# Optimization experiments

Measured on AMD Instinct MI355X. Metric: run time of the kernel, lower is better.

## Reference

```python
import jax, jax.numpy as jnp
import numpy as np

WL = 8  # word length passed to block_quantize_nearest


def block_quantize_nearest(x, wl=WL):
    """QPyTorch block_quantize_nearest with dim=0.

    One shared exponent per row (block = row of x.view(N, -1)).
    Equivalent math to the CUDA kernel: base exponent e = floor(log2(max|row|)),
    quantization step = 2^(e + 2 - wl), round-half-up in the rebased bit space.
    """
    flat = x.reshape(x.shape[0], -1)
    max_abs = jnp.max(jnp.abs(flat), axis=1, keepdims=True)  # [N, 1]
    tiny = jnp.asarray(np.finfo(np.float32).tiny, x.dtype)
    exp = jnp.floor(jnp.log2(jnp.maximum(max_abs, tiny)))
    step = jnp.exp2(exp + 2.0 - wl)                          # [N, 1]
    q = jnp.floor(flat / step + 0.5) * step                  # round-half-up
    q = jnp.where(max_abs > 0, q, flat)                      # all-zero rows pass through
    return q.reshape(x.shape)


def setup_inputs() -> dict:
    key = jax.random.key(0)
    k1, k2, k3 = jax.random.split(key, 3)
    B, D_IN, D_OUT = 8192, 4096, 4096
    x = jax.random.normal(k1, (B, D_IN), dtype=jnp.float32)
    # nn.Linear init scale ~ 1/sqrt(fan_in)
    W = jax.random.normal(k2, (D_OUT, D_IN), dtype=jnp.float32) * (1.0 / np.sqrt(D_IN))
    b = jax.random.normal(k3, (D_OUT,), dtype=jnp.float32) * (1.0 / np.sqrt(D_IN))
    return {"x": x, "W": W, "b": b}


def reference(x, W, b):
    # Linear: y = x @ W^T + b  (x already 2D, flatten(1) is identity)
    h = jnp.einsum('bi,oi->bo', x.reshape(x.shape[0], -1), W) + b
    q = block_quantize_nearest(h, WL)
    return jax.nn.relu(q)
```

## Files before the change

### kernel.cpp

```cpp
#include <hip/hip_runtime.h>

#define M 8192
#define N 4096
#define K 4096
#define BM 256
#define BN 256
#define BK 64
#define NKT (K / BK)
#define NIT (NKT / 2)

typedef __attribute__((ext_vector_type(8))) short bf16x8;
typedef __attribute__((ext_vector_type(4))) short bf16x4;
typedef __attribute__((ext_vector_type(4))) float f32x4;
typedef __attribute__((address_space(1))) const unsigned GU;
typedef __attribute__((address_space(3))) unsigned LU;

__device__ __forceinline__ unsigned short f2bf(float f) {
    unsigned u = __float_as_uint(f);
    u += 0x7fffu + ((u >> 16) & 1u);
    return (unsigned short)(u >> 16);
}

__global__ __launch_bounds__(256) void cvt_bf16_2(
    const float* __restrict__ s1, unsigned short* __restrict__ d1, int n1_4,
    const float* __restrict__ s2, unsigned short* __restrict__ d2, int n2_4,
    int* __restrict__ rowmax)
{
    if (blockIdx.x < 32) rowmax[(blockIdx.x << 8) | threadIdx.x] = 0;

    const int span = gridDim.x * blockDim.x;
    const int tid  = blockIdx.x * blockDim.x + threadIdx.x;
    const int total = n1_4 + n2_4;

    for (int base = tid; base < total; base += 4 * span) {
        f32x4 v[4];
        #pragma unroll
        for (int j = 0; j < 4; ++j) {
            const int i = base + j * span;
            const f32x4* p = (i < n1_4) ? ((const f32x4*)s1) + i
                                        : ((const f32x4*)s2) + (i - n1_4);
            v[j] = *p;
        }
        #pragma unroll
        for (int j = 0; j < 4; ++j) {
            const int i = base + j * span;
            bf16x4 o;
            #pragma unroll
            for (int k = 0; k < 4; ++k) o[k] = (short)f2bf(v[j][k]);
            bf16x4* q = (i < n1_4) ? ((bf16x4*)d1) + i : ((bf16x4*)d2) + (i - n1_4);
            *q = o;
        }
    }
}

#define BAR()   __builtin_amdgcn_s_barrier()
#define LGKM0() do { asm volatile("s_waitcnt lgkmcnt(0)" ::: "memory"); \
                     __builtin_amdgcn_sched_barrier(0); } while (0)
#define LGKM8() asm volatile("s_waitcnt lgkmcnt(8)" ::: "memory")
#define VM6()   asm volatile("s_waitcnt vmcnt(6)" ::: "memory")

#define QUAD(AR, BR, MOFF, NOFF)                                               \
    do {                                                                       \
        __builtin_amdgcn_s_setprio(1);                                         \
        _Pragma("unroll")                                                      \
        for (int m_ = 0; m_ < 4; ++m_) {                                       \
            _Pragma("unroll")                                                  \
            for (int n_ = 0; n_ < 2; ++n_) {                                   \
                acc[MOFF + m_][NOFF + n_] =                                    \
                    __builtin_amdgcn_mfma_f32_16x16x32_bf16(                   \
                        AR[m_][0], BR[n_][0], acc[MOFF + m_][NOFF + n_], 0, 0, 0); \
                acc[MOFF + m_][NOFF + n_] =                                    \
                    __builtin_amdgcn_mfma_f32_16x16x32_bf16(                   \
                        AR[m_][1], BR[n_][1], acc[MOFF + m_][NOFF + n_], 0, 0, 0); \
            }                                                                  \
        }                                                                      \
        __builtin_amdgcn_s_setprio(0);                                         \
    } while (0)

__global__ __launch_bounds__(512, 2) void gemm_bf16(
    const unsigned short* __restrict__ xb, const unsigned short* __restrict__ wb,
    const float* __restrict__ bias, float* __restrict__ out,
    int* __restrict__ rowmax)
{
    __shared__ __align__(16) short smem[65536];

    const int bid = blockIdx.x;
    const int tm = bid % (M / BM);
    const int tn = bid / (M / BM);
    const int bm = tm * BM, bn = tn * BN;

    const int t    = threadIdx.x;
    const int w_id = t >> 6;
    const int l    = t & 63;
    const int wr   = w_id >> 2;
    const int wc   = w_id & 3;
    const int lr   = l & 15;
    const int g    = l >> 4;

    const int srow_l = l >> 2;
    const int scol_l = ((l & 3) * 8) ^ ((l >> 5) * 16);
    const int loff = lr * 32 + ((g * 8) ^ ((lr >> 3) << 4));

    auto stageA = [&](int buf, int h, int kt) {
        #pragma unroll
        for (int j = 0; j < 2; ++j) {
            const int s = w_id * 2 + j;
            const unsigned short* gp =
                xb + (size_t)(bm + h * 128 + (s >> 1) * 16 + srow_l) * K
                   + kt * 64 + (s & 1) * 32 + scol_l;
            __builtin_amdgcn_global_load_lds(
                (const GU*)gp, (LU*)&smem[buf * 16384 + h * 8192 + s * 512], 16, 0, 0);
        }
    };
    auto stageB = [&](int buf, int h, int kt) {
        #pragma unroll
        for (int j = 0; j < 2; ++j) {
            const int s = w_id * 2 + j;
            const unsigned short* gp =
                wb + (size_t)(bn + h * 128 + (s >> 1) * 16 + srow_l) * K
                   + kt * 64 + (s & 1) * 32 + scol_l;
            __builtin_amdgcn_global_load_lds(
                (const GU*)gp, (LU*)&smem[32768 + buf * 16384 + h * 8192 + s * 512], 16, 0, 0);
        }
    };
    auto ldA = [&](int buf, int m, int ks) -> bf16x8 {
        return *(const bf16x8*)&smem[buf * 16384 + wr * 8192 + (m * 2 + ks) * 512 + loff];
    };
    auto ldB = [&](int buf, int n, int ks) -> bf16x8 {
        return *(const bf16x8*)&smem[32768 + buf * 16384 + (wc >> 1) * 8192 +
                                     (((wc & 1) * 4 + n) * 2 + ks) * 512 + loff];
    };

    f32x4 acc[8][4];
    #pragma unroll
    for (int m = 0; m < 8; ++m)
        #pragma unroll
        for (int n = 0; n < 4; ++n)
            acc[m][n] = (f32x4){0.f, 0.f, 0.f, 0.f};

    bf16x8 a03[4][2], a47[4][2], b01[2][2], b23[2][2];

    stageB(0, 0, 0); stageB(0, 1, 0); stageA(0, 0, 0); stageA(0, 1, 0);
    stageB(1, 0, 1); stageB(1, 1, 1); stageA(1, 0, 1);
    VM6();
    BAR();

    for (int it = 0; it < NIT; ++it) {
        const int t1  = 2 * it + 1;
        const int tp0 = (2 * it + 2) & (NKT - 1);
        const int tp1 = (2 * it + 3) & (NKT - 1);

        #pragma unroll
        for (int m = 0; m < 4; ++m) { a03[m][0] = ldA(0, m, 0); a03[m][1] = ldA(0, m, 1); }
        #pragma unroll
        for (int n = 0; n < 2; ++n) { b01[n][0] = ldB(0, n, 0); b01[n][1] = ldB(0, n, 1); }
        stageA(1, 1, t1);
        LGKM8();
        BAR(); LGKM0();
        QUAD(a03, b01, 0, 0);
        BAR();

        #pragma unroll
        for (int n = 0; n < 2; ++n) { b23[n][0] = ldB(0, 2 + n, 0); b23[n][1] = ldB(0, 2 + n, 1); }
        stageB(0, 0, tp0);
        BAR(); LGKM0();
        QUAD(a03, b23, 0, 2);
        BAR();

        #pragma unroll
        for (int m = 0; m < 4; ++m) { a47[m][0] = ldA(0, 4 + m, 0); a47[m][1] = ldA(0, 4 + m, 1); }
        stageB(0, 1, tp0);
        BAR(); LGKM0();
        QUAD(a47, b23, 4, 2);
        BAR();

        stageA(0, 0, tp0);
        BAR(); LGKM0();
        QUAD(a47, b01, 4, 0);
        VM6();
        BAR();

        #pragma unroll
        for (int m = 0; m < 4; ++m) { a03[m][0] = ldA(1, m, 0); a03[m][1] = ldA(1, m, 1); }
        #pragma unroll
        for (int n = 0; n < 2; ++n) { b01[n][0] = ldB(1, n, 0); b01[n][1] = ldB(1, n, 1); }
        stageA(0, 1, tp0);
        LGKM8();
        BAR(); LGKM0();
        QUAD(a03, b01, 0, 0);
        BAR();

        #pragma unroll
        for (int n = 0; n < 2; ++n) { b23[n][0] = ldB(1, 2 + n, 0); b23[n][1] = ldB(1, 2 + n, 1); }
        stageB(1, 0, tp1);
        BAR(); LGKM0();
        QUAD(a03, b23, 0, 2);
        BAR();

        #pragma unroll
        for (int m = 0; m < 4; ++m) { a47[m][0] = ldA(1, 4 + m, 0); a47[m][1] = ldA(1, 4 + m, 1); }
        stageB(1, 1, tp1);
        BAR(); LGKM0();
        QUAD(a47, b23, 4, 2);
        BAR();

        stageA(1, 0, tp1);
        BAR(); LGKM0();
        QUAD(a47, b01, 4, 0);
        VM6();
        BAR();
    }

    __syncthreads();

    float bv[4];
    #pragma unroll
    for (int n = 0; n < 4; ++n)
        bv[n] = bias[bn + wc * 64 + n * 16 + lr];

    #pragma unroll
    for (int m = 0; m < 8; ++m) {
        #pragma unroll
        for (int r = 0; r < 4; ++r) {
            const int row = bm + wr * 128 + m * 16 + g * 4 + r;
            float amax = 0.f;
            #pragma unroll
            for (int n = 0; n < 4; ++n) {
                acc[m][n][r] += bv[n];
                amax = fmaxf(amax, fabsf(acc[m][n][r]));
            }
            #pragma unroll
            for (int off = 1; off < 16; off <<= 1)
                amax = fmaxf(amax, __shfl_xor(amax, off));
            if (lr == 0)
                atomicMax(rowmax + row, __float_as_int(amax));
        }
    }

    float* hs = (float*)smem;
    #pragma unroll
    for (int p = 0; p < 2; ++p) {
        if (p) __syncthreads();
        if (wr == p) {
            #pragma unroll
            for (int m = 0; m < 8; ++m)
                #pragma unroll
                for (int r = 0; r < 4; ++r)
                    #pragma unroll
                    for (int n = 0; n < 4; ++n)
                        hs[(m * 16 + g * 4 + r) * 256 + wc * 64 + n * 16 + lr] =
                            acc[m][n][r];
        }
        __syncthreads();
        #pragma unroll
        for (int j = 0; j < 16; ++j) {
            const int fi  = j * 2048 + t * 4;
            const int row = fi >> 8;
            const int col = fi & 255;
            *(f32x4*)&out[(size_t)(bm + p * 128 + row) * N + bn + col] =
                *(const f32x4*)&hs[fi];
        }
    }
}

__global__ __launch_bounds__(256) void quant_relu(
    float* __restrict__ y, const int* __restrict__ rowmax)
{
    const int nvec = (M * N) / 4;
    const int span = gridDim.x * blockDim.x;
    const int tid  = blockIdx.x * blockDim.x + threadIdx.x;

    for (int base = tid; base < nvec; base += 4 * span) {
        f32x4 v[4];
        unsigned mb[4];
        #pragma unroll
        for (int j = 0; j < 4; ++j)
            v[j] = ((const f32x4*)y)[base + j * span];
        #pragma unroll
        for (int j = 0; j < 4; ++j)
            mb[j] = (unsigned)rowmax[(base + j * span) >> 10];
        #pragma unroll
        for (int j = 0; j < 4; ++j) {
            const unsigned eb   = mb[j] & 0x7f800000u;
            const float    step = __uint_as_float(eb - 0x03000000u);
            const float    inv  = __uint_as_float(0x82000000u - eb);
            f32x4 q;
            #pragma unroll
            for (int k = 0; k < 4; ++k) {
                const float qq = floorf(v[j][k] * inv + 0.5f) * step;
                q[k] = fmaxf(mb[j] ? qq : v[j][k], 0.f);
            }
            ((f32x4*)y)[base + j * span] = q;
        }
    }
}

extern "C" void kernel_launch(void* const* d_in, const int* in_sizes, int n_in,
                              void* d_out, int out_size, void* d_ws, size_t ws_size,
                              hipStream_t stream) {
    const float* x = (const float*)d_in[0];
    const float* w = (const float*)d_in[1];
    const float* b = (const float*)d_in[2];
    float* out = (float*)d_out;

    const size_t XB = (size_t)M * K * 2;
    const size_t WB = (size_t)N * K * 2;

    unsigned short* xb = (unsigned short*)d_ws;
    unsigned short* wb = (unsigned short*)((char*)d_ws + XB);
    int* rowmax        = (int*)((char*)d_ws + XB + WB);

    cvt_bf16_2<<<3072, 256, 0, stream>>>(x, xb, (M * K) / 4, w, wb, (N * K) / 4, rowmax);
    gemm_bf16<<<dim3((M / BM) * (N / BN)), 512, 0, stream>>>(xb, wb, b, out, rowmax);
    quant_relu<<<2048, 256, 0, stream>>>(out, rowmax);
}
```

Measured before the change: 532.2 us.

## Fuse quant-ReLU into GEMM via cooperative grid sync with two tiles per block

Replaces the separate GEMM and quant_relu launches with one cooperative kernel of 256 persistent blocks. Each block computes two N-tiles, stores the first, keeps the second in registers across a grid-wide sync, then quantizes the second in registers and re-reads only the first tile to quantize it. This removes one full read-modify-write pass over the 128 MB output and one launch. In exchange it adds a grid barrier, serializes two tiles per block, and rereads half the output.

```diff
diff --git a/kernel.cpp b/kernel.cpp
--- a/kernel.cpp
+++ b/kernel.cpp
@@ -1,4 +1,7 @@
 #include <hip/hip_runtime.h>
+#include <hip/hip_cooperative_groups.h>
+
+namespace cg = cooperative_groups;
 
 #define M 8192
 #define N 4096
@@ -21,6 +24,14 @@
     return (unsigned short)(u >> 16);
 }
 
+__device__ __forceinline__ float quant1(float v, unsigned mb) {
+    const unsigned eb   = mb & 0x7f800000u;
+    const float    step = __uint_as_float(eb - 0x03000000u);
+    const float    inv  = __uint_as_float(0x82000000u - eb);
+    const float    qq   = floorf(v * inv + 0.5f) * step;
+    return fmaxf(mb ? qq : v, 0.f);
+}
+
 __global__ __launch_bounds__(256) void cvt_bf16_2(
     const float* __restrict__ s1, unsigned short* __restrict__ d1, int n1_4,
     const float* __restrict__ s2, unsigned short* __restrict__ d2, int n2_4,
@@ -58,6 +69,7 @@
                      __builtin_amdgcn_sched_barrier(0); } while (0)
 #define LGKM8() asm volatile("s_waitcnt lgkmcnt(8)" ::: "memory")
 #define VM6()   asm volatile("s_waitcnt vmcnt(6)" ::: "memory")
+#define VM0()   asm volatile("s_waitcnt vmcnt(0)" ::: "memory")
 
 #define QUAD(AR, BR, MOFF, NOFF)                                               \
     do {                                                                       \
@@ -77,17 +89,12 @@
         __builtin_amdgcn_s_setprio(0);                                         \
     } while (0)
 
-__global__ __launch_bounds__(512, 2) void gemm_bf16(
+__global__ __launch_bounds__(512, 2) void gemm_fused(
     const unsigned short* __restrict__ xb, const unsigned short* __restrict__ wb,
     const float* __restrict__ bias, float* __restrict__ out,
     int* __restrict__ rowmax)
 {
     __shared__ __align__(16) short smem[65536];
-
-    const int bid = blockIdx.x;
-    const int tm = bid % (M / BM);
-    const int tn = bid / (M / BM);
-    const int bm = tm * BM, bn = tn * BN;
 
     const int t    = threadIdx.x;
     const int w_id = t >> 6;
@@ -99,198 +106,229 @@
 
     const int srow_l = l >> 2;
     const int scol_l = ((l & 3) * 8) ^ ((l >> 5) * 16);
-    const int loff = lr * 32 + ((g * 8) ^ ((lr >> 3) << 4));
-
-    auto stageA = [&](int buf, int h, int kt) {
-        #pragma unroll
-        for (int j = 0; j < 2; ++j) {
-            const int s = w_id * 2 + j;
-            const unsigned short* gp =
-                xb + (size_t)(bm + h * 128 + (s >> 1) * 16 + srow_l) * K
-                   + kt * 64 + (s & 1) * 32 + scol_l;
-            __builtin_amdgcn_global_load_lds(
-                (const GU*)gp, (LU*)&smem[buf * 16384 + h * 8192 + s * 512], 16, 0, 0);
-        }
-    };
-    auto stageB = [&](int buf, int h, int kt) {
-        #pragma unroll
-        for (int j = 0; j < 2; ++j) {
-            const int s = w_id * 2 + j;
-            const unsigned short* gp =
-                wb + (size_t)(bn + h * 128 + (s >> 1) * 16 + srow_l) * K
-                   + kt * 64 + (s & 1) * 32 + scol_l;
-            __builtin_amdgcn_global_load_lds(
-                (const GU*)gp, (LU*)&smem[32768 + buf * 16384 + h * 8192 + s * 512], 16, 0, 0);
-        }
-    };
-    auto ldA = [&](int buf, int m, int ks) -> bf16x8 {
-        return *(const bf16x8*)&smem[buf * 16384 + wr * 8192 + (m * 2 + ks) * 512 + loff];
-    };
-    auto ldB = [&](int buf, int n, int ks) -> bf16x8 {
-        return *(const bf16x8*)&smem[32768 + buf * 16384 + (wc >> 1) * 8192 +
-                                     (((wc & 1) * 4 + n) * 2 + ks) * 512 + loff];
-    };
+    const int loff   = lr * 32 + ((g * 8) ^ ((lr >> 3) << 4));
+
+    const int bid = blockIdx.x;
+    const int tm  = bid & 31;
+    const int bm  = tm * BM;
+    const int bn0 = (bid >> 5) * BN;
+    const int bn1 = bn0 + 8 * BN;
 
     f32x4 acc[8][4];
-    #pragma unroll
-    for (int m = 0; m < 8; ++m)
-        #pragma unroll
-        for (int n = 0; n < 4; ++n)
-            acc[m][n] = (f32x4){0.f, 0.f, 0.f, 0.f};
-
-    bf16x8 a03[4][2], a47[4][2], b01[2][2], b23[2][2];
-
-    stageB(0, 0, 0); stageB(0, 1, 0); stageA(0, 0, 0); stageA(0, 1, 0);
-    stageB(1, 0, 1); stageB(1, 1, 1); stageA(1, 0, 1);
-    VM6();
-    BAR();
-
-    for (int it = 0; it < NIT; ++it) {
-        const int t1  = 2 * it + 1;
-        const int tp0 = (2 * it + 2) & (NKT - 1);
-        const int tp1 = (2 * it + 3) & (NKT - 1);
-
-        #pragma unroll
-        for (int m = 0; m < 4; ++m) { a03[m][0] = ldA(0, m, 0); a03[m][1] = ldA(0, m, 1); }
-        #pragma unroll
-        for (int n = 0; n < 2; ++n) { b01[n][0] = ldB(0, n, 0); b01[n][1] = ldB(0, n, 1); }
-        stageA(1, 1, t1);
-        LGKM8();
-        BAR(); LGKM0();
-        QUAD(a03, b01, 0, 0);
-        BAR();
-
-        #pragma unroll
-        for (int n = 0; n < 2; ++n) { b23[n][0] = ldB(0, 2 + n, 0); b23[n][1] = ldB(0, 2 + n, 1); }
-        stageB(0, 0, tp0);
-        BAR(); LGKM0();
-        QUAD(a03, b23, 0, 2);
-        BAR();
-
-        #pragma unroll
-        for (int m = 0; m < 4; ++m) { a47[m][0] = ldA(0, 4 + m, 0); a47[m][1] = ldA(0, 4 + m, 1); }
-        stageB(0, 1, tp0);
-        BAR(); LGKM0();
-        QUAD(a47, b23, 4, 2);
-        BAR();
-
-        stageA(0, 0, tp0);
-        BAR(); LGKM0();
-        QUAD(a47, b01, 4, 0);
+
+    auto run_tile = [&](const unsigned short* gA, const unsigned short* gB) {
+        __syncthreads();
+        #pragma unroll
+        for (int m = 0; m < 8; ++m)
+            #pragma unroll
+            for (int n = 0; n < 4; ++n)
+                acc[m][n] = (f32x4){0.f, 0.f, 0.f, 0.f};
+
+        auto stageA = [&](int buf, int h, int kt) {
+            #pragma unroll
+            for (int j = 0; j < 2; ++j) {
+                const int s = w_id * 2 + j;
+                const unsigned short* gp =
+                    gA + (size_t)(h * 128 + (s >> 1) * 16 + srow_l) * K
+                       + kt * 64 + (s & 1) * 32 + scol_l;
+                __builtin_amdgcn_global_load_lds(
+                    (const GU*)gp, (LU*)&smem[buf * 16384 + h * 8192 + s * 512], 16, 0, 0);
+            }
+        };
+        auto stageB = [&](int buf, int h, int kt) {
+            #pragma unroll
+            for (int j = 0; j < 2; ++j) {
+                const int s = w_id * 2 + j;
+                const unsigned short* gp =
+                    gB + (size_t)(h * 128 + (s >> 1) * 16 + srow_l) * K
+                       + kt * 64 + (s & 1) * 32 + scol_l;
+                __builtin_amdgcn_global_load_lds(
+                    (const GU*)gp,
+                    (LU*)&smem[32768 + buf * 16384 + h * 8192 + s * 512], 16, 0, 0);
+            }
+        };
+        auto ldA = [&](int buf, int m, int ks) -> bf16x8 {
+            return *(const bf16x8*)&smem[buf * 16384 + wr * 8192 + (m * 2 + ks) * 512 + loff];
+        };
+        auto ldB = [&](int buf, int n, int ks) -> bf16x8 {
+            return *(const bf16x8*)&smem[32768 + buf * 16384 + (wc >> 1) * 8192 +
+                                         (((wc & 1) * 4 + n) * 2 + ks) * 512 + loff];
+        };
+
+        bf16x8 a03[4][2], a47[4][2], b01[2][2], b23[2][2];
+
+        stageB(0, 0, 0); stageB(0, 1, 0); stageA(0, 0, 0); stageA(0, 1, 0);
+        stageB(1, 0, 1); stageB(1, 1, 1); stageA(1, 0, 1);
         VM6();
         BAR();
 
-        #pragma unroll
-        for (int m = 0; m < 4; ++m) { a03[m][0] = ldA(1, m, 0); a03[m][1] = ldA(1, m, 1); }
-        #pragma unroll
-        for (int n = 0; n < 2; ++n) { b01[n][0] = ldB(1, n, 0); b01[n][1] = ldB(1, n, 1); }
-        stageA(0, 1, tp0);
-        LGKM8();
-        BAR(); LGKM0();
-        QUAD(a03, b01, 0, 0);
-        BAR();
-
-        #pragma unroll
-        for (int n = 0; n < 2; ++n) { b23[n][0] = ldB(1, 2 + n, 0); b23[n][1] = ldB(1, 2 + n, 1); }
-        stageB(1, 0, tp1);
-        BAR(); LGKM0();
-        QUAD(a03, b23, 0, 2);
-        BAR();
-
-        #pragma unroll
-        for (int m = 0; m < 4; ++m) { a47[m][0] = ldA(1, 4 + m, 0); a47[m][1] = ldA(1, 4 + m, 1); }
-        stageB(1, 1, tp1);
-        BAR(); LGKM0();
-        QUAD(a47, b23, 4, 2);
-        BAR();
-
-        stageA(1, 0, tp1);
-        BAR(); LGKM0();
-        QUAD(a47, b01, 4, 0);
-        VM6();
-        BAR();
-    }
-
-    __syncthreads();
-
-    float bv[4];
-    #pragma unroll
-    for (int n = 0; n < 4; ++n)
-        bv[n] = bias[bn + wc * 64 + n * 16 + lr];
+        for (int it = 0; it < NIT; ++it) {
+            const int t1  = 2 * it + 1;
+            const int tp0 = (2 * it + 2) & (NKT - 1);
+            const int tp1 = (2 * it + 3) & (NKT - 1);
+
+            #pragma unroll
+            for (int m = 0; m < 4; ++m) { a03[m][0] = ldA(0, m, 0); a03[m][1] = ldA(0, m, 1); }
+            #pragma unroll
+            for (int n = 0; n < 2; ++n) { b01[n][0] = ldB(0, n, 0); b01[n][1] = ldB(0, n, 1); }
+            stageA(1, 1, t1);
+            LGKM8();
+            BAR(); LGKM0();
+            QUAD(a03, b01, 0, 0);
+            BAR();
+
+            #pragma unroll
+            for (int n = 0; n < 2; ++n) { b23[n][0] = ldB(0, 2 + n, 0); b23[n][1] = ldB(0, 2 + n, 1); }
+            stageB(0, 0, tp0);
+            BAR(); LGKM0();
+            QUAD(a03, b23, 0, 2);
+            BAR();
+
+            #pragma unroll
+            for (int m = 0; m < 4; ++m) { a47[m][0] = ldA(0, 4 + m, 0); a47[m][1] = ldA(0, 4 + m, 1); }
+            stageB(0, 1, tp0);
+            BAR(); LGKM0();
+            QUAD(a47, b23, 4, 2);
+            BAR();
+
+            stageA(0, 0, tp0);
+            BAR(); LGKM0();
+            QUAD(a47, b01, 4, 0);
+            VM6();
+            BAR();
+
+            #pragma unroll
+            for (int m = 0; m < 4; ++m) { a03[m][0] = ldA(1, m, 0); a03[m][1] = ldA(1, m, 1); }
+            #pragma unroll
+            for (int n = 0; n < 2; ++n) { b01[n][0] = ldB(1, n, 0); b01[n][1] = ldB(1, n, 1); }
+            stageA(0, 1, tp0);
+            LGKM8();
+            BAR(); LGKM0();
+            QUAD(a03, b01, 0, 0);
+            BAR();
+
+            #pragma unroll
+            for (int n = 0; n < 2; ++n) { b23[n][0] = ldB(1, 2 + n, 0); b23[n][1] = ldB(1, 2 + n, 1); }
+            stageB(1, 0, tp1);
+            BAR(); LGKM0();
+            QUAD(a03, b23, 0, 2);
+            BAR();
+
+            #pragma unroll
+            for (int m = 0; m < 4; ++m) { a47[m][0] = ldA(1, 4 + m, 0); a47[m][1] = ldA(1, 4 + m, 1); }
+            stageB(1, 1, tp1);
+            BAR(); LGKM0();
+            QUAD(a47, b23, 4, 2);
+            BAR();
+
+            stageA(1, 0, tp1);
+            BAR(); LGKM0();
+            QUAD(a47, b01, 4, 0);
+            VM6();
+            BAR();
+        }
+
+        VM0();
+        __syncthreads();
+    };
+
+    auto rowmax_update = [&](int bm_, int bn_) {
+        float bv[4];
+        #pragma unroll
+        for (int n = 0; n < 4; ++n)
+            bv[n] = bias[bn_ + wc * 64 + n * 16 + lr];
+        #pragma unroll
+        for (int m = 0; m < 8; ++m) {
+            #pragma unroll
+            for (int r = 0; r < 4; ++r) {
+                const int row = bm_ + wr * 128 + m * 16 + g * 4 + r;
+                float amax = 0.f;
+                #pragma unroll
+                for (int n = 0; n < 4; ++n) {
+                    acc[m][n][r] += bv[n];
+                    amax = fmaxf(amax, fabsf(acc[m][n][r]));
+                }
+                #pragma unroll
+                for (int off = 1; off < 16; off <<= 1)
+                    amax = fmaxf(amax, __shfl_xor(amax, off));
+                if (lr == 0)
+                    atomicMax(rowmax + row, __float_as_int(amax));
+            }
+        }
+    };
+
+    auto store_tile = [&](int bm_, int bn_) {
+        float* hs = (float*)smem;
+        #pragma unroll
+        for (int p = 0; p < 2; ++p) {
+            if (p) __syncthreads();
+            if (wr == p) {
+                #pragma unroll
+                for (int m = 0; m < 8; ++m)
+                    #pragma unroll
+                    for (int r = 0; r < 4; ++r)
+                        #pragma unroll
+                        for (int n = 0; n < 4; ++n)
+                            hs[(m * 16 + g * 4 + r) * 256 + wc * 64 + n * 16 + lr] =
+                                acc[m][n][r];
+            }
+            __syncthreads();
+            #pragma unroll
+            for (int j = 0; j < 16; ++j) {
+                const int fi  = j * 2048 + t * 4;
+                const int row = fi >> 8;
+                const int col = fi & 255;
+                *(f32x4*)&out[(size_t)(bm_ + p * 128 + row) * N + bn_ + col] =
+                    *(const f32x4*)&hs[fi];
+            }
+        }
+    };
+
+    run_tile(xb + (size_t)bm * K, wb + (size_t)bn0 * K);
+    rowmax_update(bm, bn0);
+    store_tile(bm, bn0);
+
+    run_tile(xb + (size_t)bm * K, wb + (size_t)bn1 * K);
+    rowmax_update(bm, bn1);
+
+    __threadfence();
+    cg::this_grid().sync();
 
     #pragma unroll
     for (int m = 0; m < 8; ++m) {
         #pragma unroll
         for (int r = 0; r < 4; ++r) {
             const int row = bm + wr * 128 + m * 16 + g * 4 + r;
-            float amax = 0.f;
-            #pragma unroll
-            for (int n = 0; n < 4; ++n) {
-                acc[m][n][r] += bv[n];
-                amax = fmaxf(amax, fabsf(acc[m][n][r]));
-            }
-            #pragma unroll
-            for (int off = 1; off < 16; off <<= 1)
-                amax = fmaxf(amax, __shfl_xor(amax, off));
-            if (lr == 0)
-                atomicMax(rowmax + row, __float_as_int(amax));
+            const unsigned mb = (unsigned)__hip_atomic_load(
+                rowmax + row, __ATOMIC_RELAXED, __HIP_MEMORY_SCOPE_AGENT);
+            #pragma unroll
+            for (int n = 0; n < 4; ++n)
+                acc[m][n][r] = quant1(acc[m][n][r], mb);
         }
     }
-
-    float* hs = (float*)smem;
-    #pragma unroll
-    for (int p = 0; p < 2; ++p) {
-        if (p) __syncthreads();
-        if (wr == p) {
-            #pragma unroll
-            for (int m = 0; m < 8; ++m)
-                #pragma unroll
-                for (int r = 0; r < 4; ++r)
-                    #pragma unroll
-                    for (int n = 0; n < 4; ++n)
-                        hs[(m * 16 + g * 4 + r) * 256 + wc * 64 + n * 16 + lr] =
-                            acc[m][n][r];
-        }
-        __syncthreads();
-        #pragma unroll
-        for (int j = 0; j < 16; ++j) {
-            const int fi  = j * 2048 + t * 4;
-            const int row = fi >> 8;
-            const int col = fi & 255;
-            *(f32x4*)&out[(size_t)(bm + p * 128 + row) * N + bn + col] =
-                *(const f32x4*)&hs[fi];
-        }
-    }
-}
-
-__global__ __launch_bounds__(256) void quant_relu(
-    float* __restrict__ y, const int* __restrict__ rowmax)
-{
-    const int nvec = (M * N) / 4;
-    const int span = gridDim.x * blockDim.x;
-    const int tid  = blockIdx.x * blockDim.x + threadIdx.x;
-
-    for (int base = tid; base < nvec; base += 4 * span) {
+    __syncthreads();
+    store_tile(bm, bn1);
+
+    #pragma unroll 1
+    for (int jb = 0; jb < 32; jb += 4) {
         f32x4 v[4];
         unsigned mb[4];
-        #pragma unroll
-        for (int j = 0; j < 4; ++j)
-            v[j] = ((const f32x4*)y)[base + j * span];
-        #pragma unroll
-        for (int j = 0; j < 4; ++j)
-            mb[j] = (unsigned)rowmax[(base + j * span) >> 10];
-        #pragma unroll
-        for (int j = 0; j < 4; ++j) {
-            const unsigned eb   = mb[j] & 0x7f800000u;
-            const float    step = __uint_as_float(eb - 0x03000000u);
-            const float    inv  = __uint_as_float(0x82000000u - eb);
+        int rowv[4];
+        #pragma unroll
+        for (int jj = 0; jj < 4; ++jj) {
+            rowv[jj] = bm + (jb + jj) * 8 + (t >> 6);
+            v[jj] = *(const f32x4*)&out[(size_t)rowv[jj] * N + bn0 + (t & 63) * 4];
+        }
+        #pragma unroll
+        for (int jj = 0; jj < 4; ++jj)
+            mb[jj] = (unsigned)__hip_atomic_load(
+                rowmax + rowv[jj], __ATOMIC_RELAXED, __HIP_MEMORY_SCOPE_AGENT);
+        #pragma unroll
+        for (int jj = 0; jj < 4; ++jj) {
             f32x4 q;
             #pragma unroll
-            for (int k = 0; k < 4; ++k) {
-                const float qq = floorf(v[j][k] * inv + 0.5f) * step;
-                q[k] = fmaxf(mb[j] ? qq : v[j][k], 0.f);
-            }
-            ((f32x4*)y)[base + j * span] = q;
+            for (int k = 0; k < 4; ++k) q[k] = quant1(v[jj][k], mb[jj]);
+            *(f32x4*)&out[(size_t)rowv[jj] * N + bn0 + (t & 63) * 4] = q;
         }
     }
 }
@@ -311,6 +349,13 @@
     int* rowmax        = (int*)((char*)d_ws + XB + WB);
 
     cvt_bf16_2<<<3072, 256, 0, stream>>>(x, xb, (M * K) / 4, w, wb, (N * K) / 4, rowmax);
-    gemm_bf16<<<dim3((M / BM) * (N / BN)), 512, 0, stream>>>(xb, wb, b, out, rowmax);
-    quant_relu<<<2048, 256, 0, stream>>>(out, rowmax);
-}
+
+    const unsigned short* xbp = xb;
+    const unsigned short* wbp = wb;
+    const float* bp = b;
+    float* outp = out;
+    int* rmp = rowmax;
+    void* kargs[] = {(void*)&xbp, (void*)&wbp, (void*)&bp, (void*)&outp, (void*)&rmp};
+    hipLaunchCooperativeKernel((void*)gemm_fused, dim3(256), dim3(512),
+                               kargs, 0, stream);
+}
```

Result: slower. 618.7 us (+16.2%).
